# Performance work log

Hardware: AMD Instinct MI355X
Metric: run time of the kernel (lower is better)

## Reference

```python
import jax, jax.numpy as jnp
import numpy as np

K = 10           # neighbors (knn_graph default)
NEG_SLOPE = 0.2  # LeakyReLU slope
EPS = 1e-5       # BatchNorm eps
B, N = 2, 10000


def lrelu(x):
    return jnp.where(x >= 0, x, NEG_SLOPE * x)


def bn(x, g, b):
    # torch BatchNorm in training mode: batch stats (biased var) over all axes but channel (axis=1)
    axes = (0,) + tuple(range(2, x.ndim))
    m = jnp.mean(x, axes, keepdims=True)
    v = jnp.var(x, axes, keepdims=True)
    sh = (1, -1) + (1,) * (x.ndim - 2)
    return (x - m) / jnp.sqrt(v + EPS) * g.reshape(sh) + b.reshape(sh)


def conv(W, x):
    # 1x1 Conv2d / Conv1d, no bias
    if x.ndim == 4:
        return jnp.einsum('oc,bcnk->bonk', W, x)
    return jnp.einsum('oc,bcn->bon', W, x)


def knn_feat(x, k):
    # x: (B, C, N) -> DGCNN edge features (B, 2C, N, k)
    xx = jnp.sum(x * x, axis=1)                        # (B, N)
    inner = jnp.einsum('bcn,bcm->bnm', x, x)           # (B, N, N)
    d = xx[:, :, None] - 2.0 * inner + xx[:, None, :]  # squared pairwise dist
    _, idx = jax.lax.top_k(-d, k + 1)                  # k+1 smallest distances
    idx = idx[..., 1:]                                 # drop self -> (B, N, k)
    xt = jnp.transpose(x, (0, 2, 1))                   # (B, N, C)
    neigh = jax.vmap(lambda xb, ib: xb[ib])(xt, idx)   # (B, N, k, C)
    center = jnp.broadcast_to(xt[:, :, None, :], neigh.shape)
    feat = jnp.concatenate([neigh - center, center], axis=-1)
    return jnp.transpose(feat, (0, 3, 1, 2))           # (B, 2C, N, k)


def setup_inputs() -> dict:
    key = jax.random.key(0)
    ks = iter(jax.random.split(key, 64))

    def w(o, i):
        return jax.random.normal(next(ks), (o, i), jnp.float32) / np.float32(np.sqrt(i))

    inp = {}
    inp['points'] = jax.random.normal(next(ks), (B, 3, N), jnp.float32)
    lab_idx = jax.random.randint(next(ks), (B,), 0, 16)
    inp['label'] = jax.nn.one_hot(lab_idx, 16, dtype=jnp.float32)[:, :, None]  # (B,16,1)
    dims = [(64, 6), (64, 64), (64, 128), (64, 64), (64, 128), (1024, 192), (64, 16)]
    for i, (o, c) in enumerate(dims):
        inp[f'W{i}'] = w(o, c)
        inp[f'g{i}'] = jnp.ones((o,), jnp.float32)
        inp[f'b{i}'] = jnp.zeros((o,), jnp.float32)
    pdims = [(256, 1280), (256, 256), (128, 256), (6, 128)]
    for i, (o, c) in enumerate(pdims):
        inp[f'P{i}'] = w(o, c)
    for i, o in enumerate([256, 256, 128]):
        inp[f'pg{i}'] = jnp.ones((o,), jnp.float32)
        inp[f'pb{i}'] = jnp.zeros((o,), jnp.float32)
    return inp


def reference(points, label, W0, g0, b0, W1, g1, b1, W2, g2, b2, W3, g3, b3,
              W4, g4, b4, W5, g5, b5, W6, g6, b6, P0, P1, P2, P3,
              pg0, pb0, pg1, pb1, pg2, pb2):
    # EdgeConv block 1
    f = knn_feat(points, K)                      # (B, 6, N, K)
    f = lrelu(bn(conv(W0, f), g0, b0))
    f = lrelu(bn(conv(W1, f), g1, b1))
    x1 = jnp.max(f, axis=-1)                     # (B, 64, N)
    # EdgeConv block 2
    f = knn_feat(x1, K)                          # (B, 128, N, K)
    f = lrelu(bn(conv(W2, f), g2, b2))
    f = lrelu(bn(conv(W3, f), g3, b3))
    x2 = jnp.max(f, axis=-1)
    # EdgeConv block 3
    f = knn_feat(x2, K)
    f = lrelu(bn(conv(W4, f), g4, b4))
    x3 = jnp.max(f, axis=-1)
    # global feature
    xc = jnp.concatenate([x1, x2, x3], axis=1)   # (B, 192, N)
    gfeat = jnp.max(lrelu(bn(conv(W5, xc), g5, b5)), axis=-1, keepdims=True)  # (B,1024,1)
    lfeat = lrelu(bn(conv(W6, label), g6, b6))   # (B, 64, 1)
    glob = jnp.concatenate([gfeat, lfeat], axis=1)
    glob = jnp.broadcast_to(glob, (x1.shape[0], glob.shape[1], x1.shape[2]))  # (B,1088,N)
    h = jnp.concatenate([x1, x2, x3, glob], axis=1)  # (B, 1280, N)
    # point head (dropout inactive in eval)
    h = lrelu(bn(conv(P0, h), pg0, pb0))
    h = lrelu(bn(conv(P1, h), pg1, pb1))
    h = lrelu(bn(conv(P2, h), pg2, pb2))
    return conv(P3, h)                           # (B, num_classes, N)
```

## Files before the change

kernel.cpp:

```cpp
#include <hip/hip_runtime.h>
#include <math.h>

constexpr int B = 2;
constexpr int N = 10000;
constexpr int K = 10;
constexpr int NK = N * K;
constexpr float NEG = 0.2f;
constexpr float BN_EPS = 1e-5f;
constexpr int SB = 64;
constexpr int JS = 8;
constexpr int JT = 64;

#define DEV __device__ __forceinline__

__global__ void __launch_bounds__(256, 4)
xx_kernel(const float* __restrict__ x, long bstride, int C,
          float* __restrict__ xx) {
  int n = blockIdx.x * 256 + threadIdx.x;
  int b = blockIdx.y;
  if (n >= N) return;
  const float* xb = x + (long)b * bstride;
  float s = 0.f;
  for (int c = 0; c < C; ++c) { float v = xb[(long)c * N + n]; s += v * v; }
  xx[b * N + n] = s;
}

DEV unsigned int fkey(float d) {
  unsigned int b = __float_as_uint(d);
  return b ^ (((unsigned int)((int)b >> 31)) | 0x80000000u);
}
DEV unsigned long long pack_key(float d, unsigned int j) {
  return ((unsigned long long)fkey(d) << 32) | j;
}
DEV void topk_u64(unsigned long long (&best)[K], unsigned long long key) {
#pragma unroll
  for (int s = 0; s < K; ++s) {
    unsigned long long b = best[s];
    bool lt = key < b;
    best[s] = lt ? key : b;
    key = lt ? b : key;
  }
}
constexpr unsigned long long KEY_MAX = 0xFFFFFFFFFFFFFFFFull;

template<int C, int TJ, int PAD>
__global__ void __launch_bounds__(256, 4)
knn_partial_kernel(const float* __restrict__ x, long bstride,
                   const float* __restrict__ xx,
                   unsigned long long* __restrict__ pk) {
  __shared__ __align__(16) float sx[TJ][PAD];
  __shared__ float sxx[TJ];
  int b = blockIdx.z;
  int js = blockIdx.y;
  int q = blockIdx.x * 256 + threadIdx.x;
  bool valid = q < N;
  const int CH = (N + JS - 1) / JS;
  int jbeg = js * CH;
  int jend = min(N, jbeg + CH);
  const float* xb = x + (long)b * bstride;
  float xi[C];
  float xxi = 0.f;
  if (valid) {
#pragma unroll
    for (int c = 0; c < C; ++c) xi[c] = xb[(long)c * N + q];
    xxi = xx[b * N + q];
  }
  unsigned long long best[K];
#pragma unroll
  for (int k = 0; k < K; ++k) best[k] = KEY_MAX;

  for (int j0 = jbeg; j0 < jend; j0 += TJ) {
    int cnt = min(TJ, jend - j0);
    __syncthreads();
    for (int e = threadIdx.x; e < C * TJ; e += 256) {
      int tj = e & (TJ - 1);
      int c = e / TJ;
      sx[tj][c] = (tj < cnt) ? xb[(long)c * N + j0 + tj] : 0.f;
    }
    for (int e = threadIdx.x; e < TJ; e += 256)
      sxx[e] = (e < cnt) ? xx[b * N + j0 + e] : 0.f;
    __syncthreads();
    if (!valid) continue;
    for (int tj = 0; tj < cnt; ++tj) {
      float dot = 0.f;
#pragma unroll
      for (int c = 0; c < C; ++c) dot += xi[c] * sx[tj][c];
      float d = xxi - 2.f * dot + sxx[tj];
      int j = j0 + tj;
      if (j != q) {
        unsigned long long key = pack_key(d, (unsigned int)j);
        if (key < best[K - 1]) topk_u64(best, key);
      }
    }
  }
  if (valid) {
    long base = ((long)(b * N + q) * JS + js) * K;
#pragma unroll
    for (int k = 0; k < K; ++k) pk[base + k] = best[k];
  }
}

__global__ void __launch_bounds__(256, 4)
knn64_tiled_kernel(const float* __restrict__ x, long bstride,
                   const float* __restrict__ xx,
                   unsigned long long* __restrict__ pk) {
  __shared__ __align__(16) float smem[64 * 68 * 2 + 128];
  float* Qt = smem;
  float* JD = smem + 64 * 68;
  float* xxq = smem + 64 * 68 * 2;
  float* xxj = xxq + 64;
  int b = blockIdx.z, js = blockIdx.y, qt = blockIdx.x;
  int t = threadIdx.x;
  const float* xb = x + (long)b * bstride;
  const float* xxb = xx + b * N;
  int q0 = qt * 64;
#pragma unroll
  for (int r = 0; r < 16; ++r) {
    int e = t + r * 256;
    int q = e & 63, c = e >> 6;
    int qg = q0 + q;
    Qt[c * 68 + q] = (qg < N) ? xb[(long)c * N + qg] : 0.f;
  }
  if (t < 64) xxq[t] = (q0 + t < N) ? xxb[q0 + t] : 0.f;

  const int CH = N / JS;
  int jbeg = js * CH, jend = jbeg + CH;
  int tx = t & 15, ty = t >> 4;
  int sq = t & 63, quarter = t >> 6;

  unsigned long long best[K];
#pragma unroll
  for (int k = 0; k < K; ++k) best[k] = KEY_MAX;

  for (int jb = jbeg; jb < jend; jb += JT) {
    __syncthreads();
#pragma unroll
    for (int r = 0; r < 16; ++r) {
      int e = t + r * 256;
      int j = e & 63, c = e >> 6;
      int jg = jb + j;
      JD[c * 68 + j] = (jg < jend) ? xb[(long)c * N + jg] : 0.f;
    }
    if (t < 64) xxj[t] = (jb + t < jend) ? xxb[jb + t] : 3.4e38f;
    __syncthreads();

    float acc[4][4] = {};
#pragma unroll 4
    for (int c = 0; c < 64; ++c) {
      float4 aq = *(const float4*)&Qt[c * 68 + tx * 4];
      float4 bj = *(const float4*)&JD[c * 68 + ty * 4];
      float av[4] = {aq.x, aq.y, aq.z, aq.w};
      float bv[4] = {bj.x, bj.y, bj.z, bj.w};
#pragma unroll
      for (int i = 0; i < 4; ++i)
#pragma unroll
        for (int jj = 0; jj < 4; ++jj) acc[i][jj] += av[i] * bv[jj];
    }
    __syncthreads();

    float4 xxjv = *(const float4*)&xxj[ty * 4];
    float xjv[4] = {xxjv.x, xxjv.y, xxjv.z, xxjv.w};
    int selbase = q0 + tx * 4 - jb - ty * 4;
    float d4[4][4];
#pragma unroll
    for (int i = 0; i < 4; ++i) {
      float xq = xxq[tx * 4 + i];
#pragma unroll
      for (int jj = 0; jj < 4; ++jj) {
        float dv = xq - 2.f * acc[i][jj] + xjv[jj];
        d4[i][jj] = (selbase + i == jj) ? 3.4e38f : dv;
      }
    }
#pragma unroll
    for (int jj = 0; jj < 4; ++jj) {
      float4 sv = make_float4(d4[0][jj], d4[1][jj], d4[2][jj], d4[3][jj]);
      *(float4*)&JD[(ty * 4 + jj) * 68 + tx * 4] = sv;
    }
    __syncthreads();

#pragma unroll 4
    for (int jj = 0; jj < 16; ++jj) {
      int jl = quarter * 16 + jj;
      float dv = JD[jl * 68 + sq];
      unsigned long long key = pack_key(dv, (unsigned int)(jb + jl));
      if (key < best[K - 1]) topk_u64(best, key);
    }
  }
  __syncthreads();
  unsigned long long* mb = (unsigned long long*)smem;
#pragma unroll
  for (int k = 0; k < K; ++k) mb[(sq * 4 + quarter) * K + k] = best[k];
  __syncthreads();
  if (t < 64 && q0 + t < N) {
    unsigned long long fb[K];
#pragma unroll
    for (int k = 0; k < K; ++k) fb[k] = KEY_MAX;
    for (int s = 0; s < 4; ++s)
#pragma unroll
      for (int k = 0; k < K; ++k) {
        unsigned long long key = mb[(t * 4 + s) * K + k];
        if (key < fb[K - 1]) topk_u64(fb, key);
      }
    long base = ((long)(b * N + q0 + t) * JS + js) * K;
#pragma unroll
    for (int k = 0; k < K; ++k) pk[base + k] = fb[k];
  }
}

__global__ void __launch_bounds__(256, 4)
knn_merge_kernel(const unsigned long long* __restrict__ pk, int* __restrict__ idx) {
  int t = blockIdx.x * 256 + threadIdx.x;
  if (t >= B * N) return;
  unsigned long long best[K];
#pragma unroll
  for (int k = 0; k < K; ++k) best[k] = KEY_MAX;
  for (int s = 0; s < JS; ++s) {
    long base = ((long)t * JS + s) * K;
#pragma unroll
    for (int k = 0; k < K; ++k) {
      unsigned long long key = pk[base + k];
      if (key < best[K - 1]) topk_u64(best, key);
    }
  }
#pragma unroll
  for (int k = 0; k < K; ++k)
    idx[(long)t * K + k] = (int)(best[k] & 0xFFFFFFFFull);
}

__global__ void __launch_bounds__(256, 2)
gemm_kernel(const float* __restrict__ W, int Wld,
            const float* __restrict__ X, long xbstride,
            float* __restrict__ Y, const float* __restrict__ bias,
            int Co, int Cin, int M) {
  __shared__ __align__(16) float Wt[16][64];
  __shared__ __align__(16) float Xt[16][128];
  int b = blockIdx.z;
  int m0 = blockIdx.x * 128;
  int o0 = blockIdx.y * 64;
  const float* Xb = X + (long)b * xbstride;
  int t = threadIdx.x;
  int tx = t & 15, ty = t >> 4;
  float acc[4][8] = {};
  for (int c0 = 0; c0 < Cin; c0 += 16) {
#pragma unroll
    for (int r = 0; r < 4; ++r) {
      int e = t + r * 256;
      int o = e & 63, kc = e >> 6;
      int oo = o0 + o, cc = c0 + kc;
      Wt[kc][o] = (oo < Co && cc < Cin) ? W[(long)oo * Wld + cc] : 0.f;
    }
    {
      int kc = t >> 4, ms = (t & 15) * 8;
      int cc = c0 + kc;
      long rowbase = (long)cc * M;
      int mm = m0 + ms;
      if (cc < Cin && mm + 8 <= M) {
        *(float4*)&Xt[kc][ms] = *(const float4*)&Xb[rowbase + mm];
        *(float4*)&Xt[kc][ms + 4] = *(const float4*)&Xb[rowbase + mm + 4];
      } else {
#pragma unroll
        for (int r = 0; r < 8; ++r)
          Xt[kc][ms + r] = (cc < Cin && mm + r < M) ? Xb[rowbase + mm + r] : 0.f;
      }
    }
    __syncthreads();
#pragma unroll
    for (int kc = 0; kc < 16; ++kc) {
      float4 a = *(const float4*)&Wt[kc][ty * 4];
      float4 x0 = *(const float4*)&Xt[kc][tx * 4];
      float4 x1 = *(const float4*)&Xt[kc][64 + tx * 4];
      float av[4] = {a.x, a.y, a.z, a.w};
      float xr[8] = {x0.x, x0.y, x0.z, x0.w, x1.x, x1.y, x1.z, x1.w};
#pragma unroll
      for (int i = 0; i < 4; ++i)
#pragma unroll
        for (int j = 0; j < 8; ++j) acc[i][j] += av[i] * xr[j];
    }
    __syncthreads();
  }
#pragma unroll
  for (int i = 0; i < 4; ++i) {
    int oo = o0 + ty * 4 + i;
    if (oo >= Co) continue;
    float bv = bias ? bias[b * Co + oo] : 0.f;
    long ybase = ((long)b * Co + oo) * M;
    int mlo = m0 + tx * 4, mhi = m0 + 64 + tx * 4;
    if (mlo + 4 <= M) {
      float4 v = make_float4(acc[i][0] + bv, acc[i][1] + bv,
                             acc[i][2] + bv, acc[i][3] + bv);
      *(float4*)&Y[ybase + mlo] = v;
    } else {
#pragma unroll
      for (int j = 0; j < 4; ++j)
        if (mlo + j < M) Y[ybase + mlo + j] = acc[i][j] + bv;
    }
    if (mhi + 4 <= M) {
      float4 v = make_float4(acc[i][4] + bv, acc[i][5] + bv,
                             acc[i][6] + bv, acc[i][7] + bv);
      *(float4*)&Y[ybase + mhi] = v;
    } else {
#pragma unroll
      for (int j = 0; j < 4; ++j)
        if (mhi + j < M) Y[ybase + mhi + j] = acc[i][j + 4] + bv;
    }
  }
}

__global__ void wdiff_kernel(const float* __restrict__ W, int Wld, int Ch, int Co,
                             float* __restrict__ wmod) {
  int e = blockIdx.x * 256 + threadIdx.x;
  if (e < Co * Ch) {
    int o = e / Ch, c = e % Ch;
    wmod[e] = W[o * Wld + Ch + c] - W[o * Wld + c];
  }
}

__global__ void __launch_bounds__(256, 4)
gather_kernel(const float* __restrict__ yn, const float* __restrict__ yc,
              const int* __restrict__ idx, float* __restrict__ z) {
  long e = (long)blockIdx.x * 256 + threadIdx.x;
  const long total = (long)B * 64 * N * K;
  if (e >= total) return;
  int k = (int)(e % K);
  long t1 = e / K;
  int n = (int)(t1 % N);
  long t2 = t1 / N;
  int o = (int)(t2 % 64);
  int b = (int)(t2 / 64);
  int j = idx[((long)b * N + n) * K + k];
  z[e] = yn[((long)b * 64 + o) * N + j] + yc[((long)b * 64 + o) * N + n];
}

__global__ void __launch_bounds__(256, 4)
stats_kernel(const float* __restrict__ X, int C, int M,
             float* __restrict__ psum, float* __restrict__ psq) {
  int c = blockIdx.x, s = blockIdx.y;
  float sum = 0.f, sq = 0.f;
  for (int b = 0; b < B; ++b) {
    const float* p = X + ((long)b * C + c) * M;
    for (int m = s * 256 + threadIdx.x; m < M; m += SB * 256) {
      float v = p[m];
      sum += v; sq += v * v;
    }
  }
#pragma unroll
  for (int off = 32; off; off >>= 1) {
    sum += __shfl_down(sum, off);
    sq += __shfl_down(sq, off);
  }
  __shared__ float ls[8];
  int wid = threadIdx.x >> 6;
  if ((threadIdx.x & 63) == 0) { ls[wid] = sum; ls[4 + wid] = sq; }
  __syncthreads();
  if (threadIdx.x == 0) {
    psum[c * SB + s] = ls[0] + ls[1] + ls[2] + ls[3];
    psq[c * SB + s] = ls[4] + ls[5] + ls[6] + ls[7];
  }
}

__global__ void finalize_kernel(const float* __restrict__ psum, const float* __restrict__ psq,
                                const float* __restrict__ g, const float* __restrict__ bb,
                                float* __restrict__ scale, float* __restrict__ shift,
                                int C, float inv_n) {
  int c = blockIdx.x * 256 + threadIdx.x;
  if (c >= C) return;
  float s = 0.f, q = 0.f;
  for (int i = 0; i < SB; ++i) { s += psum[c * SB + i]; q += psq[c * SB + i]; }
  float mean = s * inv_n;
  float var = q * inv_n - mean * mean;
  float sc = g[c] * rsqrtf(var + BN_EPS);
  scale[c] = sc;
  shift[c] = bb[c] - mean * sc;
}

__global__ void __launch_bounds__(256, 4)
norm_kernel(float* __restrict__ X, const float* __restrict__ scale,
            const float* __restrict__ shift, int C, int M) {
  long e = (long)blockIdx.x * 256 + threadIdx.x;
  long total = (long)B * C * M;
  if (e >= total) return;
  int c = (int)((e / M) % C);
  float v = X[e] * scale[c] + shift[c];
  X[e] = v >= 0.f ? v : NEG * v;
}

__global__ void __launch_bounds__(256, 4)
maxk_kernel(const float* __restrict__ Z, float* __restrict__ xc, int coff) {
  long e = (long)blockIdx.x * 256 + threadIdx.x;
  if (e >= (long)B * 64 * N) return;
  int n = (int)(e % N);
  long t = e / N;
  int o = (int)(t % 64);
  int b = (int)(t / 64);
  const float* p = Z + (((long)(b * 64 + o) * N) + n) * K;
  float m = p[0];
#pragma unroll
  for (int k = 1; k < K; ++k) m = fmaxf(m, p[k]);
  xc[((long)b * 192 + coff + o) * N + n] = m;
}

__global__ void __launch_bounds__(256, 4)
gmax_kernel(const float* __restrict__ Z5, float* __restrict__ glob) {
  int r = blockIdx.x;
  int b = r >> 10, o = r & 1023;
  const float* p = Z5 + (long)r * N;
  float m = -3.4e38f;
  for (int n = threadIdx.x; n < N; n += 256) m = fmaxf(m, p[n]);
#pragma unroll
  for (int off = 32; off; off >>= 1) m = fmaxf(m, __shfl_down(m, off));
  __shared__ float ls[4];
  int wid = threadIdx.x >> 6;
  if ((threadIdx.x & 63) == 0) ls[wid] = m;
  __syncthreads();
  if (threadIdx.x == 0)
    glob[b * 1088 + o] = fmaxf(fmaxf(ls[0], ls[1]), fmaxf(ls[2], ls[3]));
}

__global__ void lfeat_kernel(const float* __restrict__ label, const float* __restrict__ W6,
                             const float* __restrict__ g6, const float* __restrict__ b6,
                             float* __restrict__ glob) {
  int o = threadIdx.x;
  if (o >= 64) return;
  float v[B];
  for (int b = 0; b < B; ++b) {
    float s = 0.f;
    for (int c = 0; c < 16; ++c) s += W6[o * 16 + c] * label[b * 16 + c];
    v[b] = s;
  }
  float mean = 0.f;
  for (int b = 0; b < B; ++b) mean += v[b];
  mean *= (1.f / B);
  float var = 0.f;
  for (int b = 0; b < B; ++b) var += (v[b] - mean) * (v[b] - mean);
  var *= (1.f / B);
  float sc = g6[o] * rsqrtf(var + BN_EPS);
  for (int b = 0; b < B; ++b) {
    float t = (v[b] - mean) * sc + b6[o];
    glob[b * 1088 + 1024 + o] = t >= 0.f ? t : NEG * t;
  }
}

__global__ void __launch_bounds__(256, 4)
bias0_kernel(const float* __restrict__ P0, const float* __restrict__ glob,
             float* __restrict__ bias0) {
  int t = blockIdx.x * 256 + threadIdx.x;
  if (t >= B * 256) return;
  int b = t >> 8, o = t & 255;
  float s = 0.f;
  for (int c = 0; c < 1088; ++c) s += P0[o * 1280 + 192 + c] * glob[b * 1088 + c];
  bias0[b * 256 + o] = s;
}

extern "C" void kernel_launch(void* const* d_in, const int* in_sizes, int n_in,
                              void* d_out, int out_size, void* d_ws, size_t ws_size,
                              hipStream_t stream) {
  const float* pts = (const float*)d_in[0];
  const float* label = (const float*)d_in[1];
  const float* Wt7[7]; const float* gt[7]; const float* bt[7];
  for (int i = 0; i < 7; ++i) {
    Wt7[i] = (const float*)d_in[2 + 3 * i];
    gt[i] = (const float*)d_in[3 + 3 * i];
    bt[i] = (const float*)d_in[4 + 3 * i];
  }
  const float* P0 = (const float*)d_in[23];
  const float* P1 = (const float*)d_in[24];
  const float* P2 = (const float*)d_in[25];
  const float* P3 = (const float*)d_in[26];
  const float* pg0 = (const float*)d_in[27]; const float* pb0 = (const float*)d_in[28];
  const float* pg1 = (const float*)d_in[29]; const float* pb1 = (const float*)d_in[30];
  const float* pg2 = (const float*)d_in[31]; const float* pb2 = (const float*)d_in[32];
  float* out = (float*)d_out;

  float* w = (float*)d_ws;
  float* xx = w;
  int* idx = (int*)(w + 20000);
  float* yn = w + 220000;
  float* yc = yn + 1280000;
  float* wmod = yc + 1280000;
  float* zA = wmod + 4096;
  float* zB = zA + 12800000;
  float* xc = zB + 12800000;
  float* z5 = xc + 3840000;
  float* glob = z5 + 20480000;
  float* bias0 = glob + 2176;
  float* psum = bias0 + 512;
  float* psq = psum + 65536;
  float* scale = psq + 65536;
  float* shift = scale + 1024;
  float* hA = zA;
  float* hB = zB;
  unsigned long long* pk = (unsigned long long*)zA;

  const long xcbs = (long)192 * N;
  const int qblocks = (N + 255) / 256;
  const int qtiles = (N + 63) / 64;

  auto gemm = [&](const float* W, int Wld, const float* X, long xbs, float* Y,
                  const float* bias, int Co, int Cin, int M) {
    dim3 g((M + 127) / 128, (Co + 63) / 64, B);
    gemm_kernel<<<g, 256, 0, stream>>>(W, Wld, X, xbs, Y, bias, Co, Cin, M);
  };
  auto bn_lrelu = [&](float* Z, int C, int M, const float* g, const float* bb) {
    stats_kernel<<<dim3(C, SB), 256, 0, stream>>>(Z, C, M, psum, psq);
    finalize_kernel<<<(C + 255) / 256, 256, 0, stream>>>(psum, psq, g, bb, scale, shift,
                                                         C, 1.f / (float)(B * M));
    long total = (long)B * C * M;
    norm_kernel<<<(int)((total + 255) / 256), 256, 0, stream>>>(Z, scale, shift, C, M);
  };
  auto knn3 = [&](const float* X, long bstride) {
    xx_kernel<<<dim3(qblocks, B), 256, 0, stream>>>(X, bstride, 3, xx);
    knn_partial_kernel<3, 256, 4><<<dim3(qblocks, JS, B), 256, 0, stream>>>(X, bstride, xx, pk);
    knn_merge_kernel<<<(B * N + 255) / 256, 256, 0, stream>>>(pk, idx);
  };
  auto knn64 = [&](const float* X, long bstride) {
    xx_kernel<<<dim3(qblocks, B), 256, 0, stream>>>(X, bstride, 64, xx);
    knn64_tiled_kernel<<<dim3(qtiles, JS, B), 256, 0, stream>>>(X, bstride, xx, pk);
    knn_merge_kernel<<<(B * N + 255) / 256, 256, 0, stream>>>(pk, idx);
  };
  auto edge_pre = [&](const float* Wconv, int Wld, int Cin, const float* X, long xbs) {
    gemm(Wconv, Wld, X, xbs, yn, nullptr, 64, Cin, N);
    wdiff_kernel<<<(64 * Cin + 255) / 256, 256, 0, stream>>>(Wconv, Wld, Cin, 64, wmod);
    gemm(wmod, Cin, X, xbs, yc, nullptr, 64, Cin, N);
    long tot = (long)B * 64 * N * K;
    gather_kernel<<<(int)((tot + 255) / 256), 256, 0, stream>>>(yn, yc, idx, zA);
  };

  knn3(pts, (long)3 * N);
  edge_pre(Wt7[0], 6, 3, pts, (long)3 * N);
  bn_lrelu(zA, 64, NK, gt[0], bt[0]);
  gemm(Wt7[1], 64, zA, (long)64 * NK, zB, nullptr, 64, 64, NK);
  bn_lrelu(zB, 64, NK, gt[1], bt[1]);
  maxk_kernel<<<(int)(((long)B * 64 * N + 255) / 256), 256, 0, stream>>>(zB, xc, 0);

  const float* x1 = xc;
  knn64(x1, xcbs);
  edge_pre(Wt7[2], 128, 64, x1, xcbs);
  bn_lrelu(zA, 64, NK, gt[2], bt[2]);
  gemm(Wt7[3], 64, zA, (long)64 * NK, zB, nullptr, 64, 64, NK);
  bn_lrelu(zB, 64, NK, gt[3], bt[3]);
  maxk_kernel<<<(int)(((long)B * 64 * N + 255) / 256), 256, 0, stream>>>(zB, xc, 64);

  const float* x2 = xc + (long)64 * N;
  knn64(x2, xcbs);
  edge_pre(Wt7[4], 128, 64, x2, xcbs);
  bn_lrelu(zA, 64, NK, gt[4], bt[4]);
  maxk_kernel<<<(int)(((long)B * 64 * N + 255) / 256), 256, 0, stream>>>(zA, xc, 128);

  gemm(Wt7[5], 192, xc, xcbs, z5, nullptr, 1024, 192, N);
  bn_lrelu(z5, 1024, N, gt[5], bt[5]);
  gmax_kernel<<<B * 1024, 256, 0, stream>>>(z5, glob);
  lfeat_kernel<<<1, 64, 0, stream>>>(label, Wt7[6], gt[6], bt[6], glob);
  bias0_kernel<<<2, 256, 0, stream>>>(P0, glob, bias0);

  gemm(P0, 1280, xc, xcbs, hA, bias0, 256, 192, N);
  bn_lrelu(hA, 256, N, pg0, pb0);
  gemm(P1, 256, hA, (long)256 * N, hB, nullptr, 256, 256, N);
  bn_lrelu(hB, 256, N, pg1, pb1);
  gemm(P2, 256, hB, (long)256 * N, hA, nullptr, 128, 256, N);
  bn_lrelu(hA, 128, N, pg2, pb2);
  gemm(P3, 128, hA, (long)128 * N, out, nullptr, 6, 128, N);
}
```

Before: 3.119 ms.

## Fuse BN-LeakyReLU into consumer GEMMs and max kernels, drop gather materialization

The BatchNorm normalize plus LeakyReLU pass is folded into the next consumer: a GEMM operand-load stage, the max-over-k kernel, or the global max kernel. The separate read-modify-write norm pass is gone. The edge-feature gather (yn[j]+yc[n]) is no longer written to a 12.8M-element buffer. Instead, statistics are computed from yn/yc directly, and the following GEMM gathers on the fly through shared-memory index tables. This trades several full-tensor memory passes for scattered gather loads inside the GEMM tile load and in the stats kernel.

```diff
diff --git a/kernel.cpp b/kernel.cpp
--- a/kernel.cpp
+++ b/kernel.cpp
@@ -227,19 +227,33 @@
     idx[(long)t * K + k] = (int)(best[k] & 0xFFFFFFFFull);
 }
 
+template<int MODE>
 __global__ void __launch_bounds__(256, 2)
-gemm_kernel(const float* __restrict__ W, int Wld,
-            const float* __restrict__ X, long xbstride,
-            float* __restrict__ Y, const float* __restrict__ bias,
-            int Co, int Cin, int M) {
+gemm_t_kernel(const float* __restrict__ W, int Wld,
+              const float* __restrict__ X, long xbstride,
+              const float* __restrict__ yc,
+              const int* __restrict__ idx,
+              const float* __restrict__ scale, const float* __restrict__ shift,
+              float* __restrict__ Y, const float* __restrict__ bias,
+              int Co, int Cin, int M) {
   __shared__ __align__(16) float Wt[16][64];
   __shared__ __align__(16) float Xt[16][128];
+  __shared__ int jn_s[128];
+  __shared__ int nn_s[128];
   int b = blockIdx.z;
   int m0 = blockIdx.x * 128;
   int o0 = blockIdx.y * 64;
-  const float* Xb = X + (long)b * xbstride;
   int t = threadIdx.x;
   int tx = t & 15, ty = t >> 4;
+  if constexpr (MODE == 2) {
+    if (t < 128) {
+      int m = m0 + t;
+      int n = 0, j = 0;
+      if (m < M) { n = m / K; j = idx[(long)b * N * K + m]; }
+      nn_s[t] = n; jn_s[t] = j;
+    }
+    __syncthreads();
+  }
   float acc[4][8] = {};
   for (int c0 = 0; c0 < Cin; c0 += 16) {
 #pragma unroll
@@ -252,16 +266,48 @@
     {
       int kc = t >> 4, ms = (t & 15) * 8;
       int cc = c0 + kc;
-      long rowbase = (long)cc * M;
       int mm = m0 + ms;
-      if (cc < Cin && mm + 8 <= M) {
-        *(float4*)&Xt[kc][ms] = *(const float4*)&Xb[rowbase + mm];
-        *(float4*)&Xt[kc][ms + 4] = *(const float4*)&Xb[rowbase + mm + 4];
+      float xv[8];
+      if constexpr (MODE == 2) {
+        const float* ynr = X + ((long)b * 64 + cc) * N;
+        const float* ycr = yc + ((long)b * 64 + cc) * N;
+        float sc = scale[cc], sh = shift[cc];
+#pragma unroll
+        for (int r = 0; r < 8; ++r) {
+          int m = mm + r;
+          float v = 0.f;
+          if (m < M) {
+            v = ynr[jn_s[ms + r]] + ycr[nn_s[ms + r]];
+            v = v * sc + sh;
+            v = v >= 0.f ? v : NEG * v;
+          }
+          xv[r] = v;
+        }
       } else {
-#pragma unroll
-        for (int r = 0; r < 8; ++r)
-          Xt[kc][ms + r] = (cc < Cin && mm + r < M) ? Xb[rowbase + mm + r] : 0.f;
+        bool okc = cc < Cin;
+        const float* Xr = X + (long)b * xbstride + (long)cc * M;
+        if (okc && mm + 8 <= M) {
+          float4 a0 = *(const float4*)&Xr[mm];
+          float4 a1 = *(const float4*)&Xr[mm + 4];
+          xv[0] = a0.x; xv[1] = a0.y; xv[2] = a0.z; xv[3] = a0.w;
+          xv[4] = a1.x; xv[5] = a1.y; xv[6] = a1.z; xv[7] = a1.w;
+        } else {
+#pragma unroll
+          for (int r = 0; r < 8; ++r)
+            xv[r] = (okc && mm + r < M) ? Xr[mm + r] : 0.f;
+        }
+        if constexpr (MODE == 1) {
+          float sc = okc ? scale[cc] : 0.f;
+          float sh = okc ? shift[cc] : 0.f;
+#pragma unroll
+          for (int r = 0; r < 8; ++r) {
+            float v = xv[r] * sc + sh;
+            xv[r] = v >= 0.f ? v : NEG * v;
+          }
+        }
       }
+      *(float4*)&Xt[kc][ms] = make_float4(xv[0], xv[1], xv[2], xv[3]);
+      *(float4*)&Xt[kc][ms + 4] = make_float4(xv[4], xv[5], xv[6], xv[7]);
     }
     __syncthreads();
 #pragma unroll
@@ -316,22 +362,6 @@
 }
 
 __global__ void __launch_bounds__(256, 4)
-gather_kernel(const float* __restrict__ yn, const float* __restrict__ yc,
-              const int* __restrict__ idx, float* __restrict__ z) {
-  long e = (long)blockIdx.x * 256 + threadIdx.x;
-  const long total = (long)B * 64 * N * K;
-  if (e >= total) return;
-  int k = (int)(e % K);
-  long t1 = e / K;
-  int n = (int)(t1 % N);
-  long t2 = t1 / N;
-  int o = (int)(t2 % 64);
-  int b = (int)(t2 / 64);
-  int j = idx[((long)b * N + n) * K + k];
-  z[e] = yn[((long)b * 64 + o) * N + j] + yc[((long)b * 64 + o) * N + n];
-}
-
-__global__ void __launch_bounds__(256, 4)
 stats_kernel(const float* __restrict__ X, int C, int M,
              float* __restrict__ psum, float* __restrict__ psq) {
   int c = blockIdx.x, s = blockIdx.y;
@@ -340,6 +370,37 @@
     const float* p = X + ((long)b * C + c) * M;
     for (int m = s * 256 + threadIdx.x; m < M; m += SB * 256) {
       float v = p[m];
+      sum += v; sq += v * v;
+    }
+  }
+#pragma unroll
+  for (int off = 32; off; off >>= 1) {
+    sum += __shfl_down(sum, off);
+    sq += __shfl_down(sq, off);
+  }
+  __shared__ float ls[8];
+  int wid = threadIdx.x >> 6;
+  if ((threadIdx.x & 63) == 0) { ls[wid] = sum; ls[4 + wid] = sq; }
+  __syncthreads();
+  if (threadIdx.x == 0) {
+    psum[c * SB + s] = ls[0] + ls[1] + ls[2] + ls[3];
+    psq[c * SB + s] = ls[4] + ls[5] + ls[6] + ls[7];
+  }
+}
+
+__global__ void __launch_bounds__(256, 4)
+stats_g_kernel(const float* __restrict__ yn, const float* __restrict__ yc,
+               const int* __restrict__ idx,
+               float* __restrict__ psum, float* __restrict__ psq) {
+  int c = blockIdx.x, s = blockIdx.y;
+  float sum = 0.f, sq = 0.f;
+  for (int b = 0; b < B; ++b) {
+    const float* ynr = yn + ((long)b * 64 + c) * N;
+    const float* ycr = yc + ((long)b * 64 + c) * N;
+    const int* ib = idx + (long)b * N * K;
+    for (int m = s * 256 + threadIdx.x; m < NK; m += SB * 256) {
+      int n = m / K;
+      float v = ynr[ib[m]] + ycr[n];
       sum += v; sq += v * v;
     }
   }
@@ -374,18 +435,8 @@
 }
 
 __global__ void __launch_bounds__(256, 4)
-norm_kernel(float* __restrict__ X, const float* __restrict__ scale,
-            const float* __restrict__ shift, int C, int M) {
-  long e = (long)blockIdx.x * 256 + threadIdx.x;
-  long total = (long)B * C * M;
-  if (e >= total) return;
-  int c = (int)((e / M) % C);
-  float v = X[e] * scale[c] + shift[c];
-  X[e] = v >= 0.f ? v : NEG * v;
-}
-
-__global__ void __launch_bounds__(256, 4)
-maxk_kernel(const float* __restrict__ Z, float* __restrict__ xc, int coff) {
+norm_maxk_kernel(const float* __restrict__ Z, const float* __restrict__ scale,
+                 const float* __restrict__ shift, float* __restrict__ xc, int coff) {
   long e = (long)blockIdx.x * 256 + threadIdx.x;
   if (e >= (long)B * 64 * N) return;
   int n = (int)(e % N);
@@ -393,19 +444,55 @@
   int o = (int)(t % 64);
   int b = (int)(t / 64);
   const float* p = Z + (((long)(b * 64 + o) * N) + n) * K;
-  float m = p[0];
-#pragma unroll
-  for (int k = 1; k < K; ++k) m = fmaxf(m, p[k]);
+  float sc = scale[o], sh = shift[o];
+  float m = -3.4e38f;
+#pragma unroll
+  for (int k = 0; k < K; ++k) {
+    float v = p[k] * sc + sh;
+    v = v >= 0.f ? v : NEG * v;
+    m = fmaxf(m, v);
+  }
   xc[((long)b * 192 + coff + o) * N + n] = m;
 }
 
 __global__ void __launch_bounds__(256, 4)
-gmax_kernel(const float* __restrict__ Z5, float* __restrict__ glob) {
+norm_maxk_g_kernel(const float* __restrict__ yn, const float* __restrict__ yc,
+                   const int* __restrict__ idx,
+                   const float* __restrict__ scale, const float* __restrict__ shift,
+                   float* __restrict__ xc, int coff) {
+  long e = (long)blockIdx.x * 256 + threadIdx.x;
+  if (e >= (long)B * 64 * N) return;
+  int n = (int)(e % N);
+  long t = e / N;
+  int o = (int)(t % 64);
+  int b = (int)(t / 64);
+  const int* ib = idx + ((long)b * N + n) * K;
+  const float* ynr = yn + ((long)b * 64 + o) * N;
+  float ycv = yc[((long)b * 64 + o) * N + n];
+  float sc = scale[o], sh = shift[o];
+  float m = -3.4e38f;
+#pragma unroll
+  for (int k = 0; k < K; ++k) {
+    float v = (ynr[ib[k]] + ycv) * sc + sh;
+    v = v >= 0.f ? v : NEG * v;
+    m = fmaxf(m, v);
+  }
+  xc[((long)b * 192 + coff + o) * N + n] = m;
+}
+
+__global__ void __launch_bounds__(256, 4)
+norm_gmax_kernel(const float* __restrict__ Z5, const float* __restrict__ scale,
+                 const float* __restrict__ shift, float* __restrict__ glob) {
   int r = blockIdx.x;
   int b = r >> 10, o = r & 1023;
   const float* p = Z5 + (long)r * N;
+  float sc = scale[o], sh = shift[o];
   float m = -3.4e38f;
-  for (int n = threadIdx.x; n < N; n += 256) m = fmaxf(m, p[n]);
+  for (int n = threadIdx.x; n < N; n += 256) {
+    float v = p[n] * sc + sh;
+    v = v >= 0.f ? v : NEG * v;
+    m = fmaxf(m, v);
+  }
 #pragma unroll
   for (int off = 32; off; off >>= 1) m = fmaxf(m, __shfl_down(m, off));
   __shared__ float ls[4];
@@ -477,7 +564,7 @@
   float* yn = w + 220000;
   float* yc = yn + 1280000;
   float* wmod = yc + 1280000;
-  float* zA = wmod + 4096;
+  float* zA = wmod + 8192;
   float* zB = zA + 12800000;
   float* xc = zB + 12800000;
   float* z5 = xc + 3840000;
@@ -498,14 +585,26 @@
   auto gemm = [&](const float* W, int Wld, const float* X, long xbs, float* Y,
                   const float* bias, int Co, int Cin, int M) {
     dim3 g((M + 127) / 128, (Co + 63) / 64, B);
-    gemm_kernel<<<g, 256, 0, stream>>>(W, Wld, X, xbs, Y, bias, Co, Cin, M);
-  };
-  auto bn_lrelu = [&](float* Z, int C, int M, const float* g, const float* bb) {
+    gemm_t_kernel<0><<<g, 256, 0, stream>>>(W, Wld, X, xbs, nullptr, nullptr,
+                                            nullptr, nullptr, Y, bias, Co, Cin, M);
+  };
+  auto gemm_n = [&](const float* W, int Wld, const float* X, long xbs, float* Y,
+                    int Co, int Cin, int M) {
+    dim3 g((M + 127) / 128, (Co + 63) / 64, B);
+    gemm_t_kernel<1><<<g, 256, 0, stream>>>(W, Wld, X, xbs, nullptr, nullptr,
+                                            scale, shift, Y, nullptr, Co, Cin, M);
+  };
+  auto gemm_gn = [&](const float* W, int Wld, float* Y) {
+    dim3 g((NK + 127) / 128, 1, B);
+    gemm_t_kernel<2><<<g, 256, 0, stream>>>(W, Wld, yn, 0, yc, idx,
+                                            scale, shift, Y, nullptr, 64, 64, NK);
+  };
+  auto finalize = [&](const float* g, const float* bb, int C, float inv_n) {
+    finalize_kernel<<<(C + 255) / 256, 256, 0, stream>>>(psum, psq, g, bb, scale,
+                                                         shift, C, inv_n);
+  };
+  auto stats = [&](const float* Z, int C, int M) {
     stats_kernel<<<dim3(C, SB), 256, 0, stream>>>(Z, C, M, psum, psq);
-    finalize_kernel<<<(C + 255) / 256, 256, 0, stream>>>(psum, psq, g, bb, scale, shift,
-                                                         C, 1.f / (float)(B * M));
-    long total = (long)B * C * M;
-    norm_kernel<<<(int)((total + 255) / 256), 256, 0, stream>>>(Z, scale, shift, C, M);
   };
   auto knn3 = [&](const float* X, long bstride) {
     xx_kernel<<<dim3(qblocks, B), 256, 0, stream>>>(X, bstride, 3, xx);
@@ -517,46 +616,51 @@
     knn64_tiled_kernel<<<dim3(qtiles, JS, B), 256, 0, stream>>>(X, bstride, xx, pk);
     knn_merge_kernel<<<(B * N + 255) / 256, 256, 0, stream>>>(pk, idx);
   };
-  auto edge_pre = [&](const float* Wconv, int Wld, int Cin, const float* X, long xbs) {
+  auto edge_pre = [&](const float* Wconv, int Wld, int Cin, const float* X, long xbs,
+                      const float* g, const float* bb) {
     gemm(Wconv, Wld, X, xbs, yn, nullptr, 64, Cin, N);
     wdiff_kernel<<<(64 * Cin + 255) / 256, 256, 0, stream>>>(Wconv, Wld, Cin, 64, wmod);
     gemm(wmod, Cin, X, xbs, yc, nullptr, 64, Cin, N);
-    long tot = (long)B * 64 * N * K;
-    gather_kernel<<<(int)((tot + 255) / 256), 256, 0, stream>>>(yn, yc, idx, zA);
-  };
+    stats_g_kernel<<<dim3(64, SB), 256, 0, stream>>>(yn, yc, idx, psum, psq);
+    finalize(g, bb, 64, 1.f / (float)(B * NK));
+  };
+  const int mk_blocks = (int)(((long)B * 64 * N + 255) / 256);
 
   knn3(pts, (long)3 * N);
-  edge_pre(Wt7[0], 6, 3, pts, (long)3 * N);
-  bn_lrelu(zA, 64, NK, gt[0], bt[0]);
-  gemm(Wt7[1], 64, zA, (long)64 * NK, zB, nullptr, 64, 64, NK);
-  bn_lrelu(zB, 64, NK, gt[1], bt[1]);
-  maxk_kernel<<<(int)(((long)B * 64 * N + 255) / 256), 256, 0, stream>>>(zB, xc, 0);
+  edge_pre(Wt7[0], 6, 3, pts, (long)3 * N, gt[0], bt[0]);
+  gemm_gn(Wt7[1], 64, zB);
+  stats(zB, 64, NK);
+  finalize(gt[1], bt[1], 64, 1.f / (float)(B * NK));
+  norm_maxk_kernel<<<mk_blocks, 256, 0, stream>>>(zB, scale, shift, xc, 0);
 
   const float* x1 = xc;
   knn64(x1, xcbs);
-  edge_pre(Wt7[2], 128, 64, x1, xcbs);
-  bn_lrelu(zA, 64, NK, gt[2], bt[2]);
-  gemm(Wt7[3], 64, zA, (long)64 * NK, zB, nullptr, 64, 64, NK);
-  bn_lrelu(zB, 64, NK, gt[3], bt[3]);
-  maxk_kernel<<<(int)(((long)B * 64 * N + 255) / 256), 256, 0, stream>>>(zB, xc, 64);
+  edge_pre(Wt7[2], 128, 64, x1, xcbs, gt[2], bt[2]);
+  gemm_gn(Wt7[3], 64, zB);
+  stats(zB, 64, NK);
+  finalize(gt[3], bt[3], 64, 1.f / (float)(B * NK));
+  norm_maxk_kernel<<<mk_blocks, 256, 0, stream>>>(zB, scale, shift, xc, 64);
 
   const float* x2 = xc + (long)64 * N;
   knn64(x2, xcbs);
-  edge_pre(Wt7[4], 128, 64, x2, xcbs);
-  bn_lrelu(zA, 64, NK, gt[4], bt[4]);
-  maxk_kernel<<<(int)(((long)B * 64 * N + 255) / 256), 256, 0, stream>>>(zA, xc, 128);
+  edge_pre(Wt7[4], 128, 64, x2, xcbs, gt[4], bt[4]);
+  norm_maxk_g_kernel<<<mk_blocks, 256, 0, stream>>>(yn, yc, idx, scale, shift, xc, 128);
 
   gemm(Wt7[5], 192, xc, xcbs, z5, nullptr, 1024, 192, N);
-  bn_lrelu(z5, 1024, N, gt[5], bt[5]);
-  gmax_kernel<<<B * 1024, 256, 0, stream>>>(z5, glob);
+  stats(z5, 1024, N);
+  finalize(gt[5], bt[5], 1024, 1.f / (float)(B * N));
+  norm_gmax_kernel<<<B * 1024, 256, 0, stream>>>(z5, scale, shift, glob);
   lfeat_kernel<<<1, 64, 0, stream>>>(label, Wt7[6], gt[6], bt[6], glob);
   bias0_kernel<<<2, 256, 0, stream>>>(P0, glob, bias0);
 
   gemm(P0, 1280, xc, xcbs, hA, bias0, 256, 192, N);
-  bn_lrelu(hA, 256, N, pg0, pb0);
-  gemm(P1, 256, hA, (long)256 * N, hB, nullptr, 256, 256, N);
-  bn_lrelu(hB, 256, N, pg1, pb1);
-  gemm(P2, 256, hB, (long)256 * N, hA, nullptr, 128, 256, N);
-  bn_lrelu(hA, 128, N, pg2, pb2);
-  gemm(P3, 128, hA, (long)128 * N, out, nullptr, 6, 128, N);
-}
+  stats(hA, 256, N);
+  finalize(pg0, pb0, 256, 1.f / (float)(B * N));
+  gemm_n(P1, 256, hA, (long)256 * N, hB, 256, 256, N);
+  stats(hB, 256, N);
+  finalize(pg1, pb1, 256, 1.f / (float)(B * N));
+  gemm_n(P2, 256, hB, (long)256 * N, hA, 128, 256, N);
+  stats(hA, 128, N);
+  finalize(pg2, pb2, 128, 1.f / (float)(B * N));
+  gemm_n(P3, 128, hA, (long)128 * N, out, 6, 128, N);
+}
```

After: 2.911 ms. 1.07x faster.
